# Optimization experiments

Hardware: AMD Instinct MI355X
Metric: run time of the kernel (lower is better)

## Reference

```python
import jax, jax.numpy as jnp
import numpy as np

B, C, H, W, NH = 8, 192, 128, 128, 6  # batch, channels, height, width, heads


def setup_inputs() -> dict:
    key = jax.random.key(0)
    ks = jax.random.split(key, 5)
    return {
        "x": jax.random.normal(ks[0], (B, C, H, W), jnp.float32),
        "w_qkv": jax.random.normal(ks[1], (3 * C, 1, 3, 3), jnp.float32) * 0.1,  # grouped conv, groups=C
        "b_qkv": jax.random.normal(ks[2], (3 * C,), jnp.float32) * 0.1,
        "temperature": jnp.ones((NH, 1, 1), jnp.float32),
        "w_out": jax.random.normal(ks[3], (C, C), jnp.float32) * 0.05,  # 1x1 conv as dense
        "b_out": jax.random.normal(ks[4], (C,), jnp.float32) * 0.05,
    }


def reference(x, w_qkv, b_qkv, temperature, w_out, b_out):
    b, c, h, w = x.shape
    nh = temperature.shape[0]
    # grouped 3x3 conv (groups = in_ch), padding=1
    qkv = jax.lax.conv_general_dilated(
        x, w_qkv, window_strides=(1, 1), padding=[(1, 1), (1, 1)],
        feature_group_count=c, dimension_numbers=("NCHW", "OIHW", "NCHW"),
    ) + b_qkv[None, :, None, None]
    q, k, v = jnp.split(qkv, 3, axis=1)  # each [b, c, h, w]

    def to_heads(t):
        return t.reshape(b, nh, c // nh, h * w)  # b head c (h w)

    q, k, v = to_heads(q), to_heads(k), to_heads(v)
    eps = 1e-12  # F.normalize default
    q = q / jnp.maximum(jnp.linalg.norm(q, axis=-1, keepdims=True), eps)
    k = k / jnp.maximum(jnp.linalg.norm(k, axis=-1, keepdims=True), eps)
    attn = jnp.einsum("bhcn,bhdn->bhcd", q, k) * temperature[None]  # [b, nh, c/nh, c/nh]
    attn = jax.nn.softmax(attn, axis=-1)
    out = jnp.einsum("bhcd,bhdn->bhcn", attn, v).reshape(b, c, h, w)
    out = jnp.einsum("oc,bchw->bohw", w_out, out) + b_out[None, :, None, None]
    return out
```

## Files before the change

### kernel.cpp

```cpp
#include <hip/hip_runtime.h>
#include <hip/hip_bf16.h>

constexpr int B   = 8;
constexpr int Cc  = 192;
constexpr int H   = 128;
constexpr int Wd  = 128;
constexpr int NH  = 6;
constexpr int HD  = 32;
constexpr int HW  = H * Wd;

typedef short s16x8 __attribute__((ext_vector_type(8)));
typedef float f32x16 __attribute__((ext_vector_type(16)));

constexpr size_t OFF_V    = 0;
constexpr size_t OFF_ATTN = 50331648ULL;
constexpr size_t OFF_SSQ  = OFF_ATTN + 196608ULL;
constexpr size_t OFF_ZERO = OFF_SSQ + 12288ULL;
constexpr size_t OFF_M    = OFF_ZERO + 256ULL;
constexpr int    N_ZERO   = (196608 + 12288 + 256) / 4;

__device__ inline unsigned short f2bf(float f) {
    __hip_bfloat16 h = __float2bfloat16(f);
    return *(unsigned short*)&h;
}

__global__ void zero_kernel(float* __restrict__ p, int n) {
    int i = blockIdx.x * 256 + threadIdx.x;
    if (i < n) p[i] = 0.f;
}

#define AS1C(p) ((const __attribute__((address_space(1))) void*)(p))
#define AS3(p)  ((__attribute__((address_space(3))) void*)(p))


__device__ __forceinline__ void ld6(const float* __restrict__ base, int r,
                                    int q8, float (&e)[6]) {
    const float* p = base + r * 40 + q8 * 4;
    float4 a = *(const float4*)p;
    float4 bq = *(const float4*)(p + 4);
    float2 cd = *(const float2*)(p + 8);
    e[0] = a.w; e[1] = bq.x; e[2] = bq.y; e[3] = bq.z; e[4] = bq.w; e[5] = cd.x;
}

__device__ __forceinline__ float conv_lds(
    const float* __restrict__ base, const float (&wr)[9], float br,
    int q8, int ch, unsigned short* __restrict__ frag)
{
    float rv[3][6];
    ld6(base, 0, q8, rv[0]);
    ld6(base, 1, q8, rv[1]);
    float ss = 0.f;
#pragma unroll
    for (int y = 0; y < 4; ++y) {
        ld6(base, y + 2, q8, rv[(y + 2) % 3]);
        const float* r0 = rv[y % 3];
        const float* r1 = rv[(y + 1) % 3];
        const float* r2 = rv[(y + 2) % 3];
        float o[4];
#pragma unroll
        for (int xx = 0; xx < 4; ++xx) {
            o[xx] = br
                + wr[0] * r0[xx] + wr[1] * r0[xx + 1] + wr[2] * r0[xx + 2]
                + wr[3] * r1[xx] + wr[4] * r1[xx + 1] + wr[5] * r1[xx + 2]
                + wr[6] * r2[xx] + wr[7] * r2[xx + 1] + wr[8] * r2[xx + 2];
        }
        ss += o[0] * o[0] + o[1] * o[1] + o[2] * o[2] + o[3] * o[3];
        ushort4 pk = make_ushort4(f2bf(o[0]), f2bf(o[1]), f2bf(o[2]), f2bf(o[3]));
        int g = 4 * y + (q8 >> 1);
        *(ushort4*)(frag + ((g * 32 + ch) << 3) + ((q8 & 1) << 2)) = pk;
    }
    return ss;
}

__global__ __launch_bounds__(256, 2) void fused_conv_qk(
    const float* __restrict__ x, const float* __restrict__ w,
    const float* __restrict__ bias, float* __restrict__ ssq,
    float* __restrict__ attn, const float* __restrict__ zbuf)
{
    const int tile = blockIdx.x, h = blockIdx.y, b = blockIdx.z;
    const int y0  = tile * 4;
    const int tid = threadIdx.x;
    const int ch  = tid >> 3, q8 = tid & 7;
    const int lane = tid & 63, wv = tid >> 6;
    const int m = lane & 31, hf = lane >> 5;

    __shared__ float xs[2][5760];
    __shared__ unsigned short qs[16 * 32 * 8];
    __shared__ unsigned short ks[16 * 32 * 8];

    const int gq0 = (h * 32) / 3;
    const int ncq = (h * 32 + 31) / 3 - gq0 + 1;
    const int gl  = (h * 32 + ch) / 3 - gq0;

    const int ocq = h * HD + ch;
    float wq[9], wk[9];
#pragma unroll
    for (int t = 0; t < 9; ++t) {
        wq[t] = w[(size_t)ocq * 9 + t];
        wk[t] = w[(size_t)(Cc + ocq) * 9 + t];
    }
    const float bq = bias[ocq], bk = bias[Cc + ocq];

    const float* sp[6];
    int cb[6];
    int i4[6];
    bool act[6];
#pragma unroll
    for (int j = 0; j < 6; ++j) {
        int i = tid + 256 * j;
        act[j] = (i < 1440);
        if (act[j]) {
            int t   = i / 720;
            int jj  = i - t * 720;
            int c   = jj / 60;
            int rem = jj - c * 60;
            int r   = rem / 10;
            int c4  = rem - r * 10;
            int cg  = (c < ncq) ? c : (ncq - 1);
            int gch = t * 64 + gq0 + cg;
            int y   = y0 - 1 + r;
            sp[j] = (y >= 0 && y < H)
                  ? x + ((size_t)b * Cc + gch) * HW + (size_t)y * Wd : nullptr;
            cb[j] = c4 * 4 - 4;
            i4[j] = i * 4;
        } else { sp[j] = nullptr; cb[j] = 0; i4[j] = 0; }
    }

    f32x16 acc;
#pragma unroll
    for (int i = 0; i < 16; ++i) acc[i] = 0.f;
    float ssq_a = 0.f, ssk_a = 0.f;

#pragma unroll
    for (int j = 0; j < 6; ++j) {
        if (!act[j]) continue;
        int col = cb[j];
        const float* src = (sp[j] != nullptr && (unsigned)col <= 124u)
                         ? sp[j] + col : zbuf;
        __builtin_amdgcn_global_load_lds(AS1C(src), AS3(&xs[0][i4[j]]), 16, 0, 0);
    }

#pragma unroll 1
    for (int s = 0; s < 4; ++s) {
        float* cur = xs[s & 1];
        __syncthreads();

        if (s < 3) {
            float* nxt = xs[(s + 1) & 1];
#pragma unroll
            for (int j = 0; j < 6; ++j) {
                if (!act[j]) continue;
                int col = (s + 1) * 32 + cb[j];
                const float* src = (sp[j] != nullptr && (unsigned)col <= 124u)
                                 ? sp[j] + col : zbuf;
                __builtin_amdgcn_global_load_lds(AS1C(src), AS3(&nxt[i4[j]]), 16, 0, 0);
            }
        }

        ssq_a += conv_lds(cur + gl * 240, wq, bq, q8, ch, qs);
        ssk_a += conv_lds(cur + 2880 + gl * 240, wk, bk, q8, ch, ks);
        __syncthreads();

#pragma unroll
        for (int cc = 0; cc < 2; ++cc) {
            int g = (wv * 2 + cc) * 2 + hf;
            s16x8 qa = *(const s16x8*)&qs[(g * 32 + m) << 3];
            s16x8 kb = *(const s16x8*)&ks[(g * 32 + m) << 3];
            acc = __builtin_amdgcn_mfma_f32_32x32x16_bf16(qa, kb, acc, 0, 0, 0);
        }
    }

    __syncthreads();
    float* sacc = (float*)qs;
    for (int i = tid; i < 1024; i += 256) sacc[i] = 0.f;
    __syncthreads();
#pragma unroll
    for (int r = 0; r < 16; ++r) {
        int row = (r & 3) + 8 * (r >> 2) + 4 * hf;
        atomicAdd(&sacc[row * 32 + m], acc[r]);
    }
    __syncthreads();
    float* ap = attn + (size_t)(b * NH + h) * 1024;
    for (int i = tid; i < 1024; i += 256) atomicAdd(&ap[i], sacc[i]);

    for (int off = 4; off; off >>= 1) {
        ssq_a += __shfl_down(ssq_a, off, 8);
        ssk_a += __shfl_down(ssk_a, off, 8);
    }
    if (q8 == 0) {
        atomicAdd(&ssq[b * Cc + ocq], ssq_a);
        atomicAdd(&ssq[B * Cc + b * Cc + ocq], ssk_a);
    }
}

constexpr int TS = 16;

__global__ __launch_bounds__(256) void conv_v(
    const float* __restrict__ x, const float* __restrict__ w,
    const float* __restrict__ bias, unsigned short* __restrict__ vws)
{
    int tile = blockIdx.x;
    int gv   = blockIdx.y;
    int b    = blockIdx.z;
    int y0   = tile * TS;

    __shared__ float sm[TS + 2][132];

    const float* xp = x + ((size_t)b * Cc + 128 + gv) * HW;
    for (int i = threadIdx.x; i < (TS + 2) * 32; i += 256) {
        int r = i >> 5, c4 = (i & 31) * 4;
        int y = y0 - 1 + r;
        if (y >= 0 && y < H) {
            float4 v4 = *(const float4*)(xp + (size_t)y * Wd + c4);
            sm[r][c4 + 1] = v4.x; sm[r][c4 + 2] = v4.y;
            sm[r][c4 + 3] = v4.z; sm[r][c4 + 4] = v4.w;
        } else {
            sm[r][c4 + 1] = 0.f; sm[r][c4 + 2] = 0.f;
            sm[r][c4 + 3] = 0.f; sm[r][c4 + 4] = 0.f;
        }
    }
    for (int i = threadIdx.x; i < (TS + 2) * 2; i += 256) {
        int r = i >> 1;
        sm[r][(i & 1) ? 129 : 0] = 0.f;
    }
    __syncthreads();

    float wreg[3][9], breg[3];
    for (int j = 0; j < 3; ++j) {
        const float* wp = w + (size_t)(2 * Cc + 3 * gv + j) * 9;
#pragma unroll
        for (int t = 0; t < 9; ++t) wreg[j][t] = wp[t];
        breg[j] = bias[2 * Cc + 3 * gv + j];
    }

    int xq = (threadIdx.x & 31) * 4;
    int ys = threadIdx.x >> 5;

    for (int yy = ys; yy < TS; yy += 8) {
        float rvv[3][6];
        for (int r = 0; r < 3; ++r) {
            float4 a4 = *(const float4*)&sm[yy + r][xq];
            float2 a2 = *(const float2*)&sm[yy + r][xq + 4];
            rvv[r][0] = a4.x; rvv[r][1] = a4.y; rvv[r][2] = a4.z;
            rvv[r][3] = a4.w; rvv[r][4] = a2.x; rvv[r][5] = a2.y;
        }
        for (int j = 0; j < 3; ++j) {
            unsigned short pk[4];
            for (int xx = 0; xx < 4; ++xx) {
                float s = breg[j]
                    + wreg[j][0] * rvv[0][xx] + wreg[j][1] * rvv[0][xx + 1] + wreg[j][2] * rvv[0][xx + 2]
                    + wreg[j][3] * rvv[1][xx] + wreg[j][4] * rvv[1][xx + 1] + wreg[j][5] * rvv[1][xx + 2]
                    + wreg[j][6] * rvv[2][xx] + wreg[j][7] * rvv[2][xx + 1] + wreg[j][8] * rvv[2][xx + 2];
                pk[xx] = f2bf(s);
            }
            unsigned short* op = vws + ((size_t)b * Cc + 3 * gv + j) * HW
                                     + (size_t)(y0 + yy) * Wd + xq;
            *(ushort4*)op = make_ushort4(pk[0], pk[1], pk[2], pk[3]);
        }
    }
}

__global__ void softmax_attn(float* __restrict__ attn,
                             const float* __restrict__ ssq,
                             const float* __restrict__ temp)
{
    int h = blockIdx.x % NH, b = blockIdx.x / NH;
    __shared__ float nk[32];
    if (threadIdx.x < 32)
        nk[threadIdx.x] = fmaxf(sqrtf(ssq[B * Cc + b * Cc + h * 32 + threadIdx.x]), 1e-12f);
    __syncthreads();
    int c = threadIdx.x;
    if (c >= 32) return;
    float nq = fmaxf(sqrtf(ssq[b * Cc + h * 32 + c]), 1e-12f);
    float t = temp[h];
    float* ap = attn + ((size_t)(b * NH + h) * 32 + c) * 32;
    float row[32];
    float mx = -1e30f;
    for (int d = 0; d < 32; ++d) {
        float v = ap[d] / (nq * nk[d]) * t;
        row[d] = v;
        mx = fmaxf(mx, v);
    }
    float sum = 0.f;
    for (int d = 0; d < 32; ++d) { row[d] = expf(row[d] - mx); sum += row[d]; }
    float inv = 1.f / sum;
    for (int d = 0; d < 32; ++d) ap[d] = row[d] * inv;
}

__global__ __launch_bounds__(256) void make_m(
    const float* __restrict__ attn, const float* __restrict__ w_out,
    unsigned short* __restrict__ M)
{
    int h = blockIdx.x, b = blockIdx.y;
    __shared__ float as[32][33];
    for (int i = threadIdx.x; i < 1024; i += 256)
        as[i / 32][i % 32] = attn[(size_t)((b * NH + h) * 32 + i / 32) * 32 + i % 32];
    __syncthreads();
    for (int i = threadIdx.x; i < Cc * 32; i += 256) {
        int o = i / 32, d = i % 32;
        const float* wp = w_out + (size_t)o * Cc + h * 32;
        float s = 0.f;
        for (int cp = 0; cp < 32; ++cp) s += wp[cp] * as[cp][d];
        M[((size_t)b * Cc + o) * Cc + h * 32 + d] = f2bf(s);
    }
}

constexpr int BN = 128;

__global__ __launch_bounds__(256, 3) void out_gemm(
    const unsigned short* __restrict__ vws, const unsigned short* __restrict__ M,
    const float* __restrict__ b_out, float* __restrict__ out)
{
    int n0 = blockIdx.x * BN;
    int b  = blockIdx.y;

    const unsigned short* vp = vws + (size_t)b * Cc * HW;
    const unsigned short* mp = M + (size_t)b * Cc * Cc;

    __shared__ unsigned short vs[Cc][BN];

    int tid  = threadIdx.x;
    int lane = tid & 63, wv = tid >> 6;
    int wm = wv & 1, wn = wv >> 1;
    int col = lane & 31, half = lane >> 5;

    {
        int c0 = wv * 48;
        const unsigned short* sb = vp + (size_t)(c0 + (lane >> 4)) * HW
                                      + n0 + (lane & 15) * 8;
#pragma unroll
        for (int t = 0; t < 12; ++t) {
            __builtin_amdgcn_global_load_lds(AS1C(sb + (size_t)(4 * t) * HW),
                                             AS3(&vs[c0 + 4 * t][0]), 16, 0, 0);
        }
    }
    __syncthreads();

    f32x16 acc[6];
#pragma unroll
    for (int t = 0; t < 6; ++t)
#pragma unroll
        for (int i = 0; i < 16; ++i) acc[t][i] = 0.f;

    const int nn0 = wn * 64 + col;
    const unsigned short* mrow[3];
#pragma unroll
    for (int mt = 0; mt < 3; ++mt)
        mrow[mt] = mp + (size_t)(wm * 96 + mt * 32 + col) * Cc + half * 8;

#pragma unroll 2
    for (int k0 = 0; k0 < Cc; k0 += 16) {
        s16x8 af[3];
#pragma unroll
        for (int mt = 0; mt < 3; ++mt)
            af[mt] = *(const s16x8*)(mrow[mt] + k0);

        union { s16x8 v8; unsigned short u[8]; } b0, b1;
#pragma unroll
        for (int j = 0; j < 8; ++j) {
            b0.u[j] = vs[k0 + half * 8 + j][nn0];
            b1.u[j] = vs[k0 + half * 8 + j][nn0 + 32];
        }

#pragma unroll
        for (int mt = 0; mt < 3; ++mt) {
            acc[mt * 2 + 0] = __builtin_amdgcn_mfma_f32_32x32x16_bf16(
                af[mt], b0.v8, acc[mt * 2 + 0], 0, 0, 0);
            acc[mt * 2 + 1] = __builtin_amdgcn_mfma_f32_32x32x16_bf16(
                af[mt], b1.v8, acc[mt * 2 + 1], 0, 0, 0);
        }
    }

#pragma unroll
    for (int mt = 0; mt < 3; ++mt)
#pragma unroll
        for (int nt = 0; nt < 2; ++nt) {
            int n = n0 + wn * 64 + nt * 32 + col;
#pragma unroll
            for (int r = 0; r < 16; ++r) {
                int row = (r & 3) + 8 * (r >> 2) + 4 * half;
                int o = wm * 96 + mt * 32 + row;
                out[((size_t)b * Cc + o) * HW + n] = acc[mt * 2 + nt][r] + b_out[o];
            }
        }
}

extern "C" void kernel_launch(void* const* d_in, const int* in_sizes, int n_in,
                              void* d_out, int out_size, void* d_ws, size_t ws_size,
                              hipStream_t stream) {
    const float* x      = (const float*)d_in[0];
    const float* w_qkv  = (const float*)d_in[1];
    const float* b_qkv  = (const float*)d_in[2];
    const float* temp   = (const float*)d_in[3];
    const float* w_out  = (const float*)d_in[4];
    const float* b_out  = (const float*)d_in[5];
    float* out = (float*)d_out;

    char* ws = (char*)d_ws;
    unsigned short* vws = (unsigned short*)(ws + OFF_V);
    float* attn         = (float*)(ws + OFF_ATTN);
    float* ssq          = (float*)(ws + OFF_SSQ);
    const float* zbuf   = (const float*)(ws + OFF_ZERO);
    unsigned short* M   = (unsigned short*)(ws + OFF_M);

    zero_kernel<<<(N_ZERO + 255) / 256, 256, 0, stream>>>(attn, N_ZERO);
    fused_conv_qk<<<dim3(H / 4, NH, B), 256, 0, stream>>>(x, w_qkv, b_qkv, ssq, attn, zbuf);
    conv_v<<<dim3(H / TS, 64, B), 256, 0, stream>>>(x, w_qkv, b_qkv, vws);
    softmax_attn<<<B * NH, 64, 0, stream>>>(attn, ssq, temp);
    make_m<<<dim3(NH, B), 256, 0, stream>>>(attn, w_out, M);
    out_gemm<<<dim3(HW / BN, B), 256, 0, stream>>>(vws, M, b_out, out);
}
```

Baseline: 293.5 us.

## Halve conv_qk LDS staging for higher occupancy, swizzle fragments, fuse softmax into make_m

The fused q/k conv kernel now stages the q and k input channels in separate alternating phases (8 phases instead of 4), which halves the LDS staging buffer. It also raises the launch bound from 2 to 4 blocks per CU so more waves can hide memory latency. The bf16 fragment writes and MFMA reads use a rotated channel index to cut LDS bank conflicts. The softmax and make_m kernels are merged into one launch, removing one kernel and an attn round trip through global memory. The cost is twice as many barrier and prefetch phases, plus possible register spilling under the tighter launch bound.

```diff
diff --git a/kernel.cpp b/kernel.cpp
--- a/kernel.cpp
+++ b/kernel.cpp
@@ -50,6 +50,7 @@
     ld6(base, 0, q8, rv[0]);
     ld6(base, 1, q8, rv[1]);
     float ss = 0.f;
+    const int ch2 = (ch + 8 * (q8 >> 1)) & 31;
 #pragma unroll
     for (int y = 0; y < 4; ++y) {
         ld6(base, y + 2, q8, rv[(y + 2) % 3]);
@@ -67,12 +68,12 @@
         ss += o[0] * o[0] + o[1] * o[1] + o[2] * o[2] + o[3] * o[3];
         ushort4 pk = make_ushort4(f2bf(o[0]), f2bf(o[1]), f2bf(o[2]), f2bf(o[3]));
         int g = 4 * y + (q8 >> 1);
-        *(ushort4*)(frag + ((g * 32 + ch) << 3) + ((q8 & 1) << 2)) = pk;
+        *(ushort4*)(frag + ((g * 32 + ch2) << 3) + ((q8 & 1) << 2)) = pk;
     }
     return ss;
 }
 
-__global__ __launch_bounds__(256, 2) void fused_conv_qk(
+__global__ __launch_bounds__(256, 4) void fused_conv_qk(
     const float* __restrict__ x, const float* __restrict__ w,
     const float* __restrict__ bias, float* __restrict__ ssq,
     float* __restrict__ attn, const float* __restrict__ zbuf)
@@ -84,7 +85,7 @@
     const int lane = tid & 63, wv = tid >> 6;
     const int m = lane & 31, hf = lane >> 5;
 
-    __shared__ float xs[2][5760];
+    __shared__ float xb[2][2880];
     __shared__ unsigned short qs[16 * 32 * 8];
     __shared__ unsigned short ks[16 * 32 * 8];
 
@@ -101,29 +102,26 @@
     }
     const float bq = bias[ocq], bk = bias[Cc + ocq];
 
-    const float* sp[6];
-    int cb[6];
-    int i4[6];
-    bool act[6];
-#pragma unroll
-    for (int j = 0; j < 6; ++j) {
+    const float* sp[3];
+    int cb[3];
+    int d4[3];
+    bool act[3];
+#pragma unroll
+    for (int j = 0; j < 3; ++j) {
         int i = tid + 256 * j;
-        act[j] = (i < 1440);
+        act[j] = (i < 720);
         if (act[j]) {
-            int t   = i / 720;
-            int jj  = i - t * 720;
-            int c   = jj / 60;
-            int rem = jj - c * 60;
+            int c   = i / 60;
+            int rem = i - c * 60;
             int r   = rem / 10;
             int c4  = rem - r * 10;
             int cg  = (c < ncq) ? c : (ncq - 1);
-            int gch = t * 64 + gq0 + cg;
             int y   = y0 - 1 + r;
             sp[j] = (y >= 0 && y < H)
-                  ? x + ((size_t)b * Cc + gch) * HW + (size_t)y * Wd : nullptr;
+                  ? x + ((size_t)b * Cc + gq0 + cg) * HW + (size_t)y * Wd : nullptr;
             cb[j] = c4 * 4 - 4;
-            i4[j] = i * 4;
-        } else { sp[j] = nullptr; cb[j] = 0; i4[j] = 0; }
+            d4[j] = i * 4;
+        } else { sp[j] = nullptr; cb[j] = 0; d4[j] = 0; }
     }
 
     f32x16 acc;
@@ -132,41 +130,47 @@
     float ssq_a = 0.f, ssk_a = 0.f;
 
 #pragma unroll
-    for (int j = 0; j < 6; ++j) {
+    for (int j = 0; j < 3; ++j) {
         if (!act[j]) continue;
         int col = cb[j];
         const float* src = (sp[j] != nullptr && (unsigned)col <= 124u)
                          ? sp[j] + col : zbuf;
-        __builtin_amdgcn_global_load_lds(AS1C(src), AS3(&xs[0][i4[j]]), 16, 0, 0);
+        __builtin_amdgcn_global_load_lds(AS1C(src), AS3(&xb[0][d4[j]]), 16, 0, 0);
     }
 
 #pragma unroll 1
-    for (int s = 0; s < 4; ++s) {
-        float* cur = xs[s & 1];
+    for (int p = 0; p < 8; ++p) {
+        const float* cur = xb[p & 1];
         __syncthreads();
 
-        if (s < 3) {
-            float* nxt = xs[(s + 1) & 1];
-#pragma unroll
-            for (int j = 0; j < 6; ++j) {
+        if (p < 7) {
+            int tn = (p + 1) & 1;
+            size_t toff = (size_t)(tn ? 64 : 0) * HW;
+            int scol = ((p + 1) >> 1) * 32;
+            float* nxt = xb[(p + 1) & 1];
+#pragma unroll
+            for (int j = 0; j < 3; ++j) {
                 if (!act[j]) continue;
-                int col = (s + 1) * 32 + cb[j];
+                int col = scol + cb[j];
                 const float* src = (sp[j] != nullptr && (unsigned)col <= 124u)
-                                 ? sp[j] + col : zbuf;
-                __builtin_amdgcn_global_load_lds(AS1C(src), AS3(&nxt[i4[j]]), 16, 0, 0);
+                                 ? sp[j] + toff + col : zbuf;
+                __builtin_amdgcn_global_load_lds(AS1C(src), AS3(&nxt[d4[j]]), 16, 0, 0);
             }
         }
 
-        ssq_a += conv_lds(cur + gl * 240, wq, bq, q8, ch, qs);
-        ssk_a += conv_lds(cur + 2880 + gl * 240, wk, bk, q8, ch, ks);
-        __syncthreads();
-
-#pragma unroll
-        for (int cc = 0; cc < 2; ++cc) {
-            int g = (wv * 2 + cc) * 2 + hf;
-            s16x8 qa = *(const s16x8*)&qs[(g * 32 + m) << 3];
-            s16x8 kb = *(const s16x8*)&ks[(g * 32 + m) << 3];
-            acc = __builtin_amdgcn_mfma_f32_32x32x16_bf16(qa, kb, acc, 0, 0, 0);
+        if ((p & 1) == 0) {
+            ssq_a += conv_lds(cur + gl * 240, wq, bq, q8, ch, qs);
+        } else {
+            ssk_a += conv_lds(cur + gl * 240, wk, bk, q8, ch, ks);
+            __syncthreads();
+#pragma unroll
+            for (int cc = 0; cc < 2; ++cc) {
+                int g = (wv * 2 + cc) * 2 + hf;
+                int pos = (m + 8 * (g & 3)) & 31;
+                s16x8 qa = *(const s16x8*)&qs[(g * 32 + pos) << 3];
+                s16x8 kb = *(const s16x8*)&ks[(g * 32 + pos) << 3];
+                acc = __builtin_amdgcn_mfma_f32_32x32x16_bf16(qa, kb, acc, 0, 0, 0);
+            }
         }
     }
 
@@ -260,43 +264,40 @@
     }
 }
 
-__global__ void softmax_attn(float* __restrict__ attn,
-                             const float* __restrict__ ssq,
-                             const float* __restrict__ temp)
-{
-    int h = blockIdx.x % NH, b = blockIdx.x / NH;
-    __shared__ float nk[32];
-    if (threadIdx.x < 32)
-        nk[threadIdx.x] = fmaxf(sqrtf(ssq[B * Cc + b * Cc + h * 32 + threadIdx.x]), 1e-12f);
-    __syncthreads();
-    int c = threadIdx.x;
-    if (c >= 32) return;
-    float nq = fmaxf(sqrtf(ssq[b * Cc + h * 32 + c]), 1e-12f);
-    float t = temp[h];
-    float* ap = attn + ((size_t)(b * NH + h) * 32 + c) * 32;
-    float row[32];
-    float mx = -1e30f;
-    for (int d = 0; d < 32; ++d) {
-        float v = ap[d] / (nq * nk[d]) * t;
-        row[d] = v;
-        mx = fmaxf(mx, v);
-    }
-    float sum = 0.f;
-    for (int d = 0; d < 32; ++d) { row[d] = expf(row[d] - mx); sum += row[d]; }
-    float inv = 1.f / sum;
-    for (int d = 0; d < 32; ++d) ap[d] = row[d] * inv;
-}
-
-__global__ __launch_bounds__(256) void make_m(
-    const float* __restrict__ attn, const float* __restrict__ w_out,
+__global__ __launch_bounds__(256) void softmax_make_m(
+    const float* __restrict__ attn, const float* __restrict__ ssq,
+    const float* __restrict__ temp, const float* __restrict__ w_out,
     unsigned short* __restrict__ M)
 {
     int h = blockIdx.x, b = blockIdx.y;
+    int tid = threadIdx.x;
+    __shared__ float nk[32];
     __shared__ float as[32][33];
-    for (int i = threadIdx.x; i < 1024; i += 256)
-        as[i / 32][i % 32] = attn[(size_t)((b * NH + h) * 32 + i / 32) * 32 + i % 32];
-    __syncthreads();
-    for (int i = threadIdx.x; i < Cc * 32; i += 256) {
+
+    if (tid < 32)
+        nk[tid] = fmaxf(sqrtf(ssq[B * Cc + b * Cc + h * 32 + tid]), 1e-12f);
+    __syncthreads();
+
+    if (tid < 32) {
+        int c = tid;
+        float nq = fmaxf(sqrtf(ssq[b * Cc + h * 32 + c]), 1e-12f);
+        float t = temp[h];
+        const float* ap = attn + ((size_t)(b * NH + h) * 32 + c) * 32;
+        float row[32];
+        float mx = -1e30f;
+        for (int d = 0; d < 32; ++d) {
+            float v = ap[d] / (nq * nk[d]) * t;
+            row[d] = v;
+            mx = fmaxf(mx, v);
+        }
+        float sum = 0.f;
+        for (int d = 0; d < 32; ++d) { row[d] = expf(row[d] - mx); sum += row[d]; }
+        float inv = 1.f / sum;
+        for (int d = 0; d < 32; ++d) as[c][d] = row[d] * inv;
+    }
+    __syncthreads();
+
+    for (int i = tid; i < Cc * 32; i += 256) {
         int o = i / 32, d = i % 32;
         const float* wp = w_out + (size_t)o * Cc + h * 32;
         float s = 0.f;
@@ -406,7 +407,6 @@
     zero_kernel<<<(N_ZERO + 255) / 256, 256, 0, stream>>>(attn, N_ZERO);
     fused_conv_qk<<<dim3(H / 4, NH, B), 256, 0, stream>>>(x, w_qkv, b_qkv, ssq, attn, zbuf);
     conv_v<<<dim3(H / TS, 64, B), 256, 0, stream>>>(x, w_qkv, b_qkv, vws);
-    softmax_attn<<<B * NH, 64, 0, stream>>>(attn, ssq, temp);
-    make_m<<<dim3(NH, B), 256, 0, stream>>>(attn, w_out, M);
+    softmax_make_m<<<dim3(NH, B), 256, 0, stream>>>(attn, ssq, temp, w_out, M);
     out_gemm<<<dim3(HW / BN, B), 256, 0, stream>>>(vws, M, b_out, out);
 }
```

Measured after the change: 311.8 us. 6.2% more time.

## Fuse softmax into make_m and shrink out_gemm tile to 64 columns

Applied to the files above, without the earlier changes.

Merges the softmax kernel into the M-construction kernel so the normalized attention stays in shared memory, removing one launch and a global round trip. The output GEMM tile width is halved from 128 to 64 columns and occupancy is raised to 4 blocks, which doubles the grid. In exchange, each wave does fewer MFMAs per M-fragment load, so M is reloaded more often relative to the work done.

```diff
diff --git a/kernel.cpp b/kernel.cpp
--- a/kernel.cpp
+++ b/kernel.cpp
@@ -260,43 +260,40 @@
     }
 }
 
-__global__ void softmax_attn(float* __restrict__ attn,
-                             const float* __restrict__ ssq,
-                             const float* __restrict__ temp)
-{
-    int h = blockIdx.x % NH, b = blockIdx.x / NH;
-    __shared__ float nk[32];
-    if (threadIdx.x < 32)
-        nk[threadIdx.x] = fmaxf(sqrtf(ssq[B * Cc + b * Cc + h * 32 + threadIdx.x]), 1e-12f);
-    __syncthreads();
-    int c = threadIdx.x;
-    if (c >= 32) return;
-    float nq = fmaxf(sqrtf(ssq[b * Cc + h * 32 + c]), 1e-12f);
-    float t = temp[h];
-    float* ap = attn + ((size_t)(b * NH + h) * 32 + c) * 32;
-    float row[32];
-    float mx = -1e30f;
-    for (int d = 0; d < 32; ++d) {
-        float v = ap[d] / (nq * nk[d]) * t;
-        row[d] = v;
-        mx = fmaxf(mx, v);
-    }
-    float sum = 0.f;
-    for (int d = 0; d < 32; ++d) { row[d] = expf(row[d] - mx); sum += row[d]; }
-    float inv = 1.f / sum;
-    for (int d = 0; d < 32; ++d) ap[d] = row[d] * inv;
-}
-
-__global__ __launch_bounds__(256) void make_m(
-    const float* __restrict__ attn, const float* __restrict__ w_out,
+__global__ __launch_bounds__(256) void softmax_make_m(
+    const float* __restrict__ attn, const float* __restrict__ ssq,
+    const float* __restrict__ temp, const float* __restrict__ w_out,
     unsigned short* __restrict__ M)
 {
     int h = blockIdx.x, b = blockIdx.y;
+    int tid = threadIdx.x;
+    __shared__ float nk[32];
     __shared__ float as[32][33];
-    for (int i = threadIdx.x; i < 1024; i += 256)
-        as[i / 32][i % 32] = attn[(size_t)((b * NH + h) * 32 + i / 32) * 32 + i % 32];
-    __syncthreads();
-    for (int i = threadIdx.x; i < Cc * 32; i += 256) {
+
+    if (tid < 32)
+        nk[tid] = fmaxf(sqrtf(ssq[B * Cc + b * Cc + h * 32 + tid]), 1e-12f);
+    __syncthreads();
+
+    if (tid < 32) {
+        int c = tid;
+        float nq = fmaxf(sqrtf(ssq[b * Cc + h * 32 + c]), 1e-12f);
+        float t = temp[h];
+        const float* ap = attn + ((size_t)(b * NH + h) * 32 + c) * 32;
+        float row[32];
+        float mx = -1e30f;
+        for (int d = 0; d < 32; ++d) {
+            float v = ap[d] / (nq * nk[d]) * t;
+            row[d] = v;
+            mx = fmaxf(mx, v);
+        }
+        float sum = 0.f;
+        for (int d = 0; d < 32; ++d) { row[d] = expf(row[d] - mx); sum += row[d]; }
+        float inv = 1.f / sum;
+        for (int d = 0; d < 32; ++d) as[c][d] = row[d] * inv;
+    }
+    __syncthreads();
+
+    for (int i = tid; i < Cc * 32; i += 256) {
         int o = i / 32, d = i % 32;
         const float* wp = w_out + (size_t)o * Cc + h * 32;
         float s = 0.f;
@@ -305,9 +302,9 @@
     }
 }
 
-constexpr int BN = 128;
-
-__global__ __launch_bounds__(256, 3) void out_gemm(
+constexpr int BN = 64;
+
+__global__ __launch_bounds__(256, 4) void out_gemm(
     const unsigned short* __restrict__ vws, const unsigned short* __restrict__ M,
     const float* __restrict__ b_out, float* __restrict__ out)
 {
@@ -326,23 +323,23 @@
 
     {
         int c0 = wv * 48;
-        const unsigned short* sb = vp + (size_t)(c0 + (lane >> 4)) * HW
-                                      + n0 + (lane & 15) * 8;
-#pragma unroll
-        for (int t = 0; t < 12; ++t) {
-            __builtin_amdgcn_global_load_lds(AS1C(sb + (size_t)(4 * t) * HW),
-                                             AS3(&vs[c0 + 4 * t][0]), 16, 0, 0);
-        }
-    }
-    __syncthreads();
-
-    f32x16 acc[6];
-#pragma unroll
-    for (int t = 0; t < 6; ++t)
+        const unsigned short* sb = vp + (size_t)(c0 + (lane >> 3)) * HW
+                                      + n0 + (lane & 7) * 8;
+#pragma unroll
+        for (int t = 0; t < 6; ++t) {
+            __builtin_amdgcn_global_load_lds(AS1C(sb + (size_t)(8 * t) * HW),
+                                             AS3(&vs[c0 + 8 * t][0]), 16, 0, 0);
+        }
+    }
+    __syncthreads();
+
+    f32x16 acc[3];
+#pragma unroll
+    for (int t = 0; t < 3; ++t)
 #pragma unroll
         for (int i = 0; i < 16; ++i) acc[t][i] = 0.f;
 
-    const int nn0 = wn * 64 + col;
+    const int nn0 = wn * 32 + col;
     const unsigned short* mrow[3];
 #pragma unroll
     for (int mt = 0; mt < 3; ++mt)
@@ -355,34 +352,27 @@
         for (int mt = 0; mt < 3; ++mt)
             af[mt] = *(const s16x8*)(mrow[mt] + k0);
 
-        union { s16x8 v8; unsigned short u[8]; } b0, b1;
-#pragma unroll
-        for (int j = 0; j < 8; ++j) {
+        union { s16x8 v8; unsigned short u[8]; } b0;
+#pragma unroll
+        for (int j = 0; j < 8; ++j)
             b0.u[j] = vs[k0 + half * 8 + j][nn0];
-            b1.u[j] = vs[k0 + half * 8 + j][nn0 + 32];
-        }
-
-#pragma unroll
-        for (int mt = 0; mt < 3; ++mt) {
-            acc[mt * 2 + 0] = __builtin_amdgcn_mfma_f32_32x32x16_bf16(
-                af[mt], b0.v8, acc[mt * 2 + 0], 0, 0, 0);
-            acc[mt * 2 + 1] = __builtin_amdgcn_mfma_f32_32x32x16_bf16(
-                af[mt], b1.v8, acc[mt * 2 + 1], 0, 0, 0);
-        }
-    }
-
-#pragma unroll
-    for (int mt = 0; mt < 3; ++mt)
-#pragma unroll
-        for (int nt = 0; nt < 2; ++nt) {
-            int n = n0 + wn * 64 + nt * 32 + col;
-#pragma unroll
-            for (int r = 0; r < 16; ++r) {
-                int row = (r & 3) + 8 * (r >> 2) + 4 * half;
-                int o = wm * 96 + mt * 32 + row;
-                out[((size_t)b * Cc + o) * HW + n] = acc[mt * 2 + nt][r] + b_out[o];
-            }
-        }
+
+#pragma unroll
+        for (int mt = 0; mt < 3; ++mt)
+            acc[mt] = __builtin_amdgcn_mfma_f32_32x32x16_bf16(
+                af[mt], b0.v8, acc[mt], 0, 0, 0);
+    }
+
+#pragma unroll
+    for (int mt = 0; mt < 3; ++mt) {
+        int n = n0 + wn * 32 + col;
+#pragma unroll
+        for (int r = 0; r < 16; ++r) {
+            int row = (r & 3) + 8 * (r >> 2) + 4 * half;
+            int o = wm * 96 + mt * 32 + row;
+            out[((size_t)b * Cc + o) * HW + n] = acc[mt][r] + b_out[o];
+        }
+    }
 }
 
 extern "C" void kernel_launch(void* const* d_in, const int* in_sizes, int n_in,
@@ -406,7 +396,6 @@
     zero_kernel<<<(N_ZERO + 255) / 256, 256, 0, stream>>>(attn, N_ZERO);
     fused_conv_qk<<<dim3(H / 4, NH, B), 256, 0, stream>>>(x, w_qkv, b_qkv, ssq, attn, zbuf);
     conv_v<<<dim3(H / TS, 64, B), 256, 0, stream>>>(x, w_qkv, b_qkv, vws);
-    softmax_attn<<<B * NH, 64, 0, stream>>>(attn, ssq, temp);
-    make_m<<<dim3(NH, B), 256, 0, stream>>>(attn, w_out, M);
+    softmax_make_m<<<dim3(NH, B), 256, 0, stream>>>(attn, ssq, temp, w_out, M);
     out_gemm<<<dim3(HW / BN, B), 256, 0, stream>>>(vws, M, b_out, out);
 }
```

After: 299.7 us. 1.02x slower.
